# Optimization experiments

Hardware: AMD Instinct MI355X
Metric: run time of the kernel (lower is better)

Reference implementation:

```python
import jax, jax.numpy as jnp
import numpy as np

N, E, F, H = 50000, 500000, 128, 128   # nodes, edges, in-features, hidden
L, R, B = 3, 8, 30                     # layers, relations, bases
G, C = 16, 8                           # graphs in batch, classes
EPS = 1e-5


def setup_inputs() -> dict:
    key = jax.random.key(0)
    ks = jax.random.split(key, 16)
    x = jax.random.normal(ks[0], (N, F), jnp.float32)
    edge_index = jax.random.randint(ks[1], (2, E), 0, N)
    edge_attr = jax.random.randint(ks[2], (E,), 0, R)
    batch = jnp.sort(jax.random.randint(ks[3], (N,), 0, G))
    # RGCN params (all layers share shapes since F == H)
    basis = jax.random.normal(ks[4], (L, B, H, H), jnp.float32) * 0.05
    comp = jax.random.normal(ks[5], (L, R, B), jnp.float32) * 0.2
    root = jax.random.normal(ks[6], (L, H, H), jnp.float32) * 0.05
    bias = jnp.zeros((L, H), jnp.float32)
    # BatchNorm (eval mode: running stats)
    bn1_gamma = jnp.ones((F,), jnp.float32)
    bn1_beta = jnp.zeros((F,), jnp.float32)
    bn1_mean = jax.random.normal(ks[7], (F,), jnp.float32) * 0.1
    bn1_var = jax.random.uniform(ks[8], (F,), jnp.float32, 0.5, 1.5)
    bn2_gamma = jnp.ones((H,), jnp.float32)
    bn2_beta = jnp.zeros((H,), jnp.float32)
    bn2_mean = jax.random.normal(ks[9], (H,), jnp.float32) * 0.1
    bn2_var = jax.random.uniform(ks[10], (H,), jnp.float32, 0.5, 1.5)
    fc1_w = jax.random.normal(ks[11], (H, H), jnp.float32) * 0.05
    fc1_b = jnp.zeros((H,), jnp.float32)
    fc2_w = jax.random.normal(ks[12], (H, C), jnp.float32) * 0.05
    fc2_b = jnp.zeros((C,), jnp.float32)
    return dict(x=x, edge_index=edge_index, edge_attr=edge_attr, batch=batch,
                bn1_gamma=bn1_gamma, bn1_beta=bn1_beta, bn1_mean=bn1_mean, bn1_var=bn1_var,
                basis=basis, comp=comp, root=root, bias=bias,
                bn2_gamma=bn2_gamma, bn2_beta=bn2_beta, bn2_mean=bn2_mean, bn2_var=bn2_var,
                fc1_w=fc1_w, fc1_b=fc1_b, fc2_w=fc2_w, fc2_b=fc2_b)


def _bn(x, gamma, beta, mean, var):
    return (x - mean) * jax.lax.rsqrt(var + EPS) * gamma + beta


def _rgcn_layer(x, basis_l, comp_l, root_l, bias_l, src, dst, edge_attr):
    # root transform + bias
    out = x @ root_l + bias_l
    # relation-wise basis-decomposed message passing, mean-aggregated per relation
    for r in range(R):
        W_r = jnp.einsum('b,bio->io', comp_l[r], basis_l)  # [H, H]
        xw = x @ W_r                                       # [N, H]
        mask = (edge_attr == r).astype(x.dtype)            # [E]
        msg = xw[src] * mask[:, None]                      # gather + mask
        agg = jax.ops.segment_sum(msg, dst, num_segments=N)
        deg = jax.ops.segment_sum(mask, dst, num_segments=N)
        out = out + agg / jnp.maximum(deg, 1.0)[:, None]
    return out


def reference(x, edge_index, edge_attr, batch,
              bn1_gamma, bn1_beta, bn1_mean, bn1_var,
              basis, comp, root, bias,
              bn2_gamma, bn2_beta, bn2_mean, bn2_var,
              fc1_w, fc1_b, fc2_w, fc2_b):
    src, dst = edge_index[0], edge_index[1]
    h = _bn(x, bn1_gamma, bn1_beta, bn1_mean, bn1_var)
    for l in range(L):
        h = jax.nn.relu(_rgcn_layer(h, basis[l], comp[l], root[l], bias[l], src, dst, edge_attr))
        # dropout is identity in eval mode
    # global mean pool per graph
    sums = jax.ops.segment_sum(h, batch, num_segments=G)            # [G, H]
    counts = jax.ops.segment_sum(jnp.ones((N,), h.dtype), batch, num_segments=G)
    g = sums / jnp.maximum(counts, 1.0)[:, None]
    g = _bn(g, bn2_gamma, bn2_beta, bn2_mean, bn2_var)
    # temporal_type == 'mean'
    v = jax.nn.relu(g.mean(axis=0))                                 # [H]
    v = jax.nn.relu(v @ fc1_w + fc1_b)
    logits = v @ fc2_w + fc2_b                                      # [C]
    return jax.nn.log_softmax(logits, axis=-1)
```

## Files before the change

### kernel.cpp

```cpp
#include <hip/hip_runtime.h>
#include <hip/hip_bf16.h>

#define NN 50000
#define NE 500000
#define HID 128
#define LAYERS 3
#define RELS 8
#define BASES 30
#define GRAPHS 16
#define CLASSES 8
#define EPSV 1e-5f
#define NOUT (HID * (RELS + 1))
#define SCAN_CHUNK 1024
#define SCAN_NBLK ((NN + SCAN_CHUNK - 1) / SCAN_CHUNK)
#define PCHUNK 128
#define NSTRIPE ((NN + 127) / 128)
#define NSG ((NSTRIPE + 7) / 8)

typedef __attribute__((ext_vector_type(8))) short short8;
typedef __attribute__((ext_vector_type(4))) float f32x4;
typedef __attribute__((ext_vector_type(2))) float f32x2;

__device__ __forceinline__ float bf2f(unsigned short u) {
    union { unsigned int i; float f; } x; x.i = ((unsigned int)u) << 16; return x.f;
}
__device__ __forceinline__ unsigned short f2bf(float f) {
    __hip_bfloat16 b = __float2bfloat16(f);
    return *(unsigned short*)&b;
}
template <bool HI>
__device__ __forceinline__ f32x2 fp8x2_2f(int u) {
    return __builtin_amdgcn_cvt_pk_f32_fp8(u, HI);
}
__device__ __forceinline__ int permf(int f) {
    return (f & 64) | ((f & 15) << 2) | ((f >> 4) & 3);
}
__device__ __forceinline__ int ipermf(int q) {
    return (q & 64) | ((q & 3) << 4) | ((q >> 2) & 15);
}

__global__ __launch_bounds__(256) void build_wcat(const float* __restrict__ basis,
                                                  const float* __restrict__ comp,
                                                  const float* __restrict__ root,
                                                  unsigned short* __restrict__ wT) {
    int bid = blockIdx.x;
    int l = bid >> 6;
    int k0 = (bid & 63) << 1;
    __shared__ float cl[RELS * BASES];
    int tid = threadIdx.x;
    if (tid < RELS * BASES) cl[tid] = comp[l * RELS * BASES + tid];
    __syncthreads();
    int j = tid & 127;
    int k = k0 + (tid >> 7);
    int pk = permf(k);
    const float* bp = basis + ((size_t)l * BASES * HID + k) * HID + j;
    float acc[RELS];
#pragma unroll
    for (int r = 0; r < RELS; ++r) acc[r] = 0.f;
    for (int b = 0; b < BASES; ++b) {
        float v = bp[(size_t)b * HID * HID];
#pragma unroll
        for (int r = 0; r < RELS; ++r) acc[r] += cl[r * BASES + b] * v;
    }
    unsigned short* wl = wT + (size_t)l * NOUT * HID;
#pragma unroll
    for (int r = 0; r < RELS; ++r)
        wl[(size_t)((1 + r) * HID + j) * HID + pk] = f2bf(acc[r]);
    wl[(size_t)j * HID + pk] = f2bf(root[((size_t)l * HID + k) * HID + j]);
}

__global__ void bn1_kernel(const float* __restrict__ x, const float* __restrict__ gamma,
                           const float* __restrict__ beta, const float* __restrict__ mean,
                           const float* __restrict__ var, unsigned short* __restrict__ habf) {
    int idx = blockIdx.x * blockDim.x + threadIdx.x;
    if (idx >= NN * HID) return;
    int q = idx & (HID - 1);
    int n = idx >> 7;
    int f = ipermf(q);
    habf[idx] = f2bf((x[(n << 7) + f] - mean[f]) * rsqrtf(var[f] + EPSV) * gamma[f] + beta[f]);
}

__global__ void deg_kernel(const int* __restrict__ ei, const int* __restrict__ ea,
                           float* __restrict__ deg) {
    int e = blockIdx.x * blockDim.x + threadIdx.x;
    if (e >= NE) return;
    int dst = ei[NE + e];
    atomicAdd(&deg[(size_t)dst * RELS + ea[e]], 1.0f);
}

__global__ void invdeg_kernel(float* __restrict__ deg, int* __restrict__ degi) {
    int n = blockIdx.x * blockDim.x + threadIdx.x;
    if (n >= NN) return;
    float s = 0.f;
#pragma unroll
    for (int r = 0; r < RELS; ++r) {
        float d = deg[(size_t)n * RELS + r];
        s += d;
        deg[(size_t)n * RELS + r] = 1.0f / fmaxf(d, 1.0f);
    }
    degi[n] = (int)(s + 0.5f);
}

__global__ __launch_bounds__(256) void scan_partial(const int* __restrict__ degi,
                                                    int* __restrict__ rowptr,
                                                    int* __restrict__ bsum) {
    __shared__ int ssc[256];
    int t = threadIdx.x;
    int base = blockIdx.x * SCAN_CHUNK + t * 4;
    int v[4];
#pragma unroll
    for (int j = 0; j < 4; ++j) v[j] = (base + j < NN) ? degi[base + j] : 0;
    int tsum = v[0] + v[1] + v[2] + v[3];
    ssc[t] = tsum;
    __syncthreads();
    for (int ofs = 1; ofs < 256; ofs <<= 1) {
        int add = (t >= ofs) ? ssc[t - ofs] : 0;
        __syncthreads();
        ssc[t] += add;
        __syncthreads();
    }
    int excl = ssc[t] - tsum;
    int e = 0;
#pragma unroll
    for (int j = 0; j < 4; ++j) {
        if (base + j < NN) rowptr[base + j] = excl + e;
        e += v[j];
    }
    if (t == 255) bsum[blockIdx.x] = ssc[255];
}

__global__ void scan_bsum(int* __restrict__ bsum) {
    if (threadIdx.x == 0) {
        int acc = 0;
        for (int b = 0; b < SCAN_NBLK; ++b) { int v = bsum[b]; bsum[b] = acc; acc += v; }
    }
}

__global__ __launch_bounds__(256) void scan_add(int* __restrict__ rowptr,
                                                const int* __restrict__ bsum) {
    int i = blockIdx.x * blockDim.x + threadIdx.x;
    if (i < NN) rowptr[i] += bsum[i >> 10];
    if (i == 0) rowptr[NN] = NE;
}

__global__ void fill_kernel(const int* __restrict__ ei, const int* __restrict__ ea,
                            const int* __restrict__ rowptr, const float* __restrict__ invdeg,
                            int* __restrict__ fillcnt, int* __restrict__ epk,
                            float* __restrict__ escale) {
    int e = blockIdx.x * blockDim.x + threadIdx.x;
    if (e >= NE) return;
    int src = ei[e];
    int dst = ei[NE + e];
    int r = ea[e];
    int pos = atomicAdd(&fillcnt[dst], 1);
    int slot = rowptr[dst] + pos;
    epk[slot] = src | (r << 20);
    escale[slot] = invdeg[(size_t)dst * RELS + r];
}

__global__ __launch_bounds__(256) void gemm_mfma(const unsigned short* __restrict__ habf,
                                                 const unsigned short* __restrict__ wT,
                                                 const float* __restrict__ bias,
                                                 unsigned short* __restrict__ hnb,
                                                 unsigned char* __restrict__ xwb) {
    __shared__ __align__(16) unsigned short As[128][72];
    __shared__ __align__(16) unsigned short Bs[128][72];
    int bid = blockIdx.x;
    int sm8 = bid & 7;
    int rest = bid >> 3;
    int n0 = rest % (RELS + 1);
    int g = rest / (RELS + 1);
    int stripe = g * 8 + sm8;
    if (stripe >= NSTRIPE) return;
    int row0 = stripe * 128;

    int tid = threadIdx.x;
    int wave = tid >> 6, lane = tid & 63;
    int wm = (wave & 1) * 64, wn = (wave >> 1) * 64;
    int quad = lane >> 4, l16 = lane & 15;

    f32x4 acc[4][4];
#pragma unroll
    for (int i = 0; i < 4; ++i)
#pragma unroll
        for (int j = 0; j < 4; ++j) acc[i][j] = (f32x4){0.f, 0.f, 0.f, 0.f};

    int srow = tid >> 1;
    int shalf = (tid & 1) * 32;
    for (int k0 = 0; k0 < HID; k0 += 64) {
        int grow = row0 + srow;
        const uint4* ga = (const uint4*)(habf + (size_t)grow * HID + k0 + shalf);
        const uint4* gb = (const uint4*)(wT + (size_t)(n0 * 128 + srow) * HID + k0 + shalf);
        uint4 z = {0u, 0u, 0u, 0u};
#pragma unroll
        for (int c = 0; c < 4; ++c) {
            *(uint4*)&As[srow][shalf + c * 8] = (grow < NN) ? ga[c] : z;
            *(uint4*)&Bs[srow][shalf + c * 8] = gb[c];
        }
        __syncthreads();
#pragma unroll
        for (int kc = 0; kc < 2; ++kc) {
            int ko = kc * 32 + quad * 8;
            short8 a[4], b[4];
#pragma unroll
            for (int i = 0; i < 4; ++i) {
                a[i] = *(const short8*)&As[wm + i * 16 + l16][ko];
                b[i] = *(const short8*)&Bs[wn + i * 16 + l16][ko];
            }
#pragma unroll
            for (int i = 0; i < 4; ++i)
#pragma unroll
                for (int j = 0; j < 4; ++j)
                    acc[i][j] = __builtin_amdgcn_mfma_f32_16x16x32_bf16(a[i], b[j], acc[i][j], 0, 0, 0);
        }
        __syncthreads();
    }

    int pbase = wn + l16 * 4;
    if (n0 == 0) {
#pragma unroll
        for (int i = 0; i < 4; ++i)
#pragma unroll
            for (int reg = 0; reg < 4; ++reg) {
                int grow = row0 + wm + i * 16 + quad * 4 + reg;
                if (grow >= NN) continue;
                unsigned lo = (unsigned)f2bf(acc[i][0][reg] + bias[wn + l16]) |
                              ((unsigned)f2bf(acc[i][1][reg] + bias[wn + 16 + l16]) << 16);
                unsigned hi = (unsigned)f2bf(acc[i][2][reg] + bias[wn + 32 + l16]) |
                              ((unsigned)f2bf(acc[i][3][reg] + bias[wn + 48 + l16]) << 16);
                uint2 pk = {lo, hi};
                *(uint2*)(hnb + (size_t)grow * HID + pbase) = pk;
            }
    } else {
        int cbase = (n0 - 1) * 128;
#pragma unroll
        for (int i = 0; i < 4; ++i)
#pragma unroll
            for (int reg = 0; reg < 4; ++reg) {
                int grow = row0 + wm + i * 16 + quad * 4 + reg;
                if (grow >= NN) continue;
                unsigned w = (unsigned)__builtin_amdgcn_cvt_pk_fp8_f32(acc[i][0][reg], acc[i][1][reg], 0, false);
                w = (unsigned)__builtin_amdgcn_cvt_pk_fp8_f32(acc[i][2][reg], acc[i][3][reg], (int)w, true);
                *(unsigned*)(xwb + (size_t)grow * (RELS * HID) + cbase + pbase) = w;
            }
    }
}

__global__ __launch_bounds__(256) void aggregate_kernel(const int* __restrict__ rowptr,
                                                        const int* __restrict__ epk,
                                                        const float* __restrict__ escale,
                                                        const unsigned char* __restrict__ xwb,
                                                        const unsigned short* __restrict__ hnb,
                                                        unsigned short* __restrict__ habf) {
    int lane = threadIdx.x & 63;
    int half = lane >> 5;
    int hl = lane & 31;
    int node = (blockIdx.x << 3) + ((threadIdx.x >> 6) << 1) + half;
    if (node >= NN) return;
    int beg = rowptr[node], end = rowptr[node + 1];
    float a0 = 0.f, a1 = 0.f, a2 = 0.f, a3 = 0.f;
    for (int b0 = beg; b0 < end; b0 += 32) {
        int cnt = min(32, end - b0);
        int myp = 0; float mys = 0.f;
        if (hl < cnt) { myp = epk[b0 + hl]; mys = escale[b0 + hl]; }
        int sbase = half << 5;
        int j = 0;
        for (; j + 2 <= cnt; j += 2) {
            int p0 = __shfl(myp, sbase + j);
            int p1 = __shfl(myp, sbase + j + 1);
            float s0 = __shfl(mys, sbase + j);
            float s1 = __shfl(mys, sbase + j + 1);
            unsigned u0 = *(const unsigned*)(xwb + (size_t)(p0 & 0xFFFFF) * (RELS * HID) + (p0 >> 20) * HID + hl * 4);
            unsigned u1 = *(const unsigned*)(xwb + (size_t)(p1 & 0xFFFFF) * (RELS * HID) + (p1 >> 20) * HID + hl * 4);
            f32x2 l0 = fp8x2_2f<false>((int)u0), h0 = fp8x2_2f<true>((int)u0);
            f32x2 l1 = fp8x2_2f<false>((int)u1), h1 = fp8x2_2f<true>((int)u1);
            a0 += l0.x * s0 + l1.x * s1;
            a1 += l0.y * s0 + l1.y * s1;
            a2 += h0.x * s0 + h1.x * s1;
            a3 += h0.y * s0 + h1.y * s1;
        }
        for (; j < cnt; ++j) {
            int p = __shfl(myp, sbase + j);
            float s = __shfl(mys, sbase + j);
            unsigned u = *(const unsigned*)(xwb + (size_t)(p & 0xFFFFF) * (RELS * HID) + (p >> 20) * HID + hl * 4);
            f32x2 lo = fp8x2_2f<false>((int)u), hi = fp8x2_2f<true>((int)u);
            a0 += lo.x * s; a1 += lo.y * s; a2 += hi.x * s; a3 += hi.y * s;
        }
    }
    const ushort2* hp = (const ushort2*)(hnb + (size_t)node * HID + hl * 4);
    ushort2 c0 = hp[0], c1 = hp[1];
    ushort2 o0, o1;
    o0.x = f2bf(fmaxf(bf2f(c0.x) + a0, 0.f));
    o0.y = f2bf(fmaxf(bf2f(c0.y) + a1, 0.f));
    o1.x = f2bf(fmaxf(bf2f(c1.x) + a2, 0.f));
    o1.y = f2bf(fmaxf(bf2f(c1.y) + a3, 0.f));
    ushort2* op = (ushort2*)(habf + (size_t)node * HID + hl * 4);
    op[0] = o0;
    op[1] = o1;
}

__global__ __launch_bounds__(256) void pool_kernel(const unsigned short* __restrict__ habf,
                                                   const int* __restrict__ batch,
                                                   float* __restrict__ psum,
                                                   float* __restrict__ pcnt) {
    int tid = threadIdx.x;
    int f = tid & 127;
    int sub = tid >> 7;
    int base = blockIdx.x * PCHUNK;
    float acc = 0.f, cnt = 0.f;
    int gcur = -1;
    for (int it = 0; it < PCHUNK / 2; ++it) {
        int node = base + it * 2 + sub;
        if (node >= NN) break;
        int g = batch[node];
        if (g != gcur) {
            if (gcur >= 0) {
                atomicAdd(&psum[gcur * HID + f], acc);
                if (f == 0) atomicAdd(&pcnt[gcur], cnt);
            }
            gcur = g; acc = 0.f; cnt = 0.f;
        }
        acc += bf2f(habf[(size_t)node * HID + f]);
        cnt += 1.f;
    }
    if (gcur >= 0) {
        atomicAdd(&psum[gcur * HID + f], acc);
        if (f == 0) atomicAdd(&pcnt[gcur], cnt);
    }
}

__global__ void head_kernel(const float* __restrict__ psum, const float* __restrict__ pcnt,
                            const float* __restrict__ g2, const float* __restrict__ b2,
                            const float* __restrict__ m2, const float* __restrict__ v2,
                            const float* __restrict__ fc1w, const float* __restrict__ fc1b,
                            const float* __restrict__ fc2w, const float* __restrict__ fc2b,
                            float* __restrict__ out) {
    __shared__ float v[HID];
    __shared__ float u[HID];
    __shared__ float lg[CLASSES];
    int j = threadIdx.x;
    int pj = permf(j);
    float acc = 0.f;
    for (int g = 0; g < GRAPHS; ++g) {
        float val = psum[g * HID + pj] / fmaxf(pcnt[g], 1.0f);
        val = (val - m2[j]) * rsqrtf(v2[j] + EPSV) * g2[j] + b2[j];
        acc += val;
    }
    v[j] = fmaxf(acc / (float)GRAPHS, 0.f);
    __syncthreads();
    float s = fc1b[j];
    for (int k = 0; k < HID; ++k) s += v[k] * fc1w[k * HID + j];
    u[j] = fmaxf(s, 0.f);
    __syncthreads();
    if (j < CLASSES) {
        float t = fc2b[j];
        for (int k = 0; k < HID; ++k) t += u[k] * fc2w[k * CLASSES + j];
        lg[j] = t;
    }
    __syncthreads();
    if (j < CLASSES) {
        float mx = lg[0];
        for (int c = 1; c < CLASSES; ++c) mx = fmaxf(mx, lg[c]);
        float se = 0.f;
        for (int c = 0; c < CLASSES; ++c) se += expf(lg[c] - mx);
        out[j] = lg[j] - mx - logf(se);
    }
}

extern "C" void kernel_launch(void* const* d_in, const int* in_sizes, int n_in,
                              void* d_out, int out_size, void* d_ws, size_t ws_size,
                              hipStream_t stream) {
    const float* x     = (const float*)d_in[0];
    const int*   ei    = (const int*)d_in[1];
    const int*   ea    = (const int*)d_in[2];
    const int*   batch = (const int*)d_in[3];
    const float* bn1g  = (const float*)d_in[4];
    const float* bn1b  = (const float*)d_in[5];
    const float* bn1m  = (const float*)d_in[6];
    const float* bn1v  = (const float*)d_in[7];
    const float* basis = (const float*)d_in[8];
    const float* comp  = (const float*)d_in[9];
    const float* root  = (const float*)d_in[10];
    const float* bias  = (const float*)d_in[11];
    const float* bn2g  = (const float*)d_in[12];
    const float* bn2b  = (const float*)d_in[13];
    const float* bn2m  = (const float*)d_in[14];
    const float* bn2v  = (const float*)d_in[15];
    const float* fc1w  = (const float*)d_in[16];
    const float* fc1b  = (const float*)d_in[17];
    const float* fc2w  = (const float*)d_in[18];
    const float* fc2b  = (const float*)d_in[19];

    float* ws = (float*)d_ws;
    size_t off = 0;
    unsigned short* wT = (unsigned short*)(ws + off); off += (size_t)LAYERS * NOUT * HID / 2;
    unsigned short* hnb  = (unsigned short*)(ws + off); off += (size_t)NN * HID / 2;
    unsigned short* habf = (unsigned short*)(ws + off); off += (size_t)NN * HID / 2;
    float* deg    = ws + off; off += (size_t)NN * RELS;
    float* psum   = ws + off; off += (size_t)GRAPHS * HID + GRAPHS;
    float* pcnt   = psum + GRAPHS * HID;
    float* escale = ws + off; off += (size_t)NE;
    int* degi     = (int*)(ws + off); off += (size_t)NN;
    int* rowptr   = (int*)(ws + off); off += (size_t)NN + 1;
    int* fillcnt  = (int*)(ws + off); off += (size_t)NN;
    int* bsum     = (int*)(ws + off); off += (size_t)SCAN_NBLK;
    int* epk      = (int*)(ws + off); off += (size_t)NE;
    off = (off + 3) & ~(size_t)3;
    unsigned char* xwb = (unsigned char*)(ws + off);
    off += (size_t)NN * RELS * HID / 4;
    if (ws_size < off * sizeof(float)) return;

    hipMemsetAsync(psum, 0, (GRAPHS * HID + GRAPHS) * sizeof(float), stream);
    hipMemsetAsync(deg, 0, (size_t)NN * RELS * sizeof(float), stream);
    hipMemsetAsync(fillcnt, 0, (size_t)NN * sizeof(int), stream);

    build_wcat<<<LAYERS * 64, 256, 0, stream>>>(basis, comp, root, wT);
    bn1_kernel<<<(NN * HID + 255) / 256, 256, 0, stream>>>(x, bn1g, bn1b, bn1m, bn1v, habf);

    deg_kernel<<<(NE + 255) / 256, 256, 0, stream>>>(ei, ea, deg);
    invdeg_kernel<<<(NN + 255) / 256, 256, 0, stream>>>(deg, degi);
    scan_partial<<<SCAN_NBLK, 256, 0, stream>>>(degi, rowptr, bsum);
    scan_bsum<<<1, 64, 0, stream>>>(bsum);
    scan_add<<<(NN + 255) / 256, 256, 0, stream>>>(rowptr, bsum);
    fill_kernel<<<(NE + 255) / 256, 256, 0, stream>>>(ei, ea, rowptr, deg, fillcnt, epk, escale);

    int gblocks = NSG * (RELS + 1) * 8;
    for (int l = 0; l < LAYERS; ++l) {
        gemm_mfma<<<gblocks, 256, 0, stream>>>(habf, wT + (size_t)l * NOUT * HID,
                                               bias + (size_t)l * HID, hnb, xwb);
        aggregate_kernel<<<(NN + 7) / 8, 256, 0, stream>>>(rowptr, epk, escale, xwb, hnb, habf);
    }

    pool_kernel<<<(NN + PCHUNK - 1) / PCHUNK, 256, 0, stream>>>(habf, batch, psum, pcnt);
    head_kernel<<<1, 128, 0, stream>>>(psum, pcnt, bn2g, bn2b, bn2m, bn2v,
                                       fc1w, fc1b, fc2w, fc2b, (float*)d_out);
}
```

Measured before the change: 433.0 us.

## Use direct global-to-LDS loads in GEMM and fetch inverse degree per relation via shuffles

The GEMM now loads the full 128x128 A and B tiles into LDS in one pass using global_load_lds with an XOR swizzle, replacing the two-step register-staged K loop and halving the barriers. The per-edge escale array is removed: each aggregation lane loads the node's per-relation inverse degree once and edges read it with a shuffle indexed by relation. The edge loop is unrolled by 4 to keep more gathers in flight. LDS use per GEMM block grows to 64 KB, which may lower occupancy, and the extra shuffles add instruction cost.

```diff
diff --git a/kernel.cpp b/kernel.cpp
--- a/kernel.cpp
+++ b/kernel.cpp
@@ -38,6 +38,11 @@
 __device__ __forceinline__ int ipermf(int q) {
     return (q & 64) | ((q & 3) << 4) | ((q >> 2) & 15);
 }
+__device__ __forceinline__ void gload16(const void* g, void* l) {
+    __builtin_amdgcn_global_load_lds(
+        (const __attribute__((address_space(1))) unsigned int*)g,
+        (__attribute__((address_space(3))) unsigned int*)l, 16, 0, 0);
+}
 
 __global__ __launch_bounds__(256) void build_wcat(const float* __restrict__ basis,
                                                   const float* __restrict__ comp,
@@ -144,18 +149,15 @@
 }
 
 __global__ void fill_kernel(const int* __restrict__ ei, const int* __restrict__ ea,
-                            const int* __restrict__ rowptr, const float* __restrict__ invdeg,
-                            int* __restrict__ fillcnt, int* __restrict__ epk,
-                            float* __restrict__ escale) {
+                            const int* __restrict__ rowptr,
+                            int* __restrict__ fillcnt, int* __restrict__ epk) {
     int e = blockIdx.x * blockDim.x + threadIdx.x;
     if (e >= NE) return;
     int src = ei[e];
     int dst = ei[NE + e];
     int r = ea[e];
     int pos = atomicAdd(&fillcnt[dst], 1);
-    int slot = rowptr[dst] + pos;
-    epk[slot] = src | (r << 20);
-    escale[slot] = invdeg[(size_t)dst * RELS + r];
+    epk[rowptr[dst] + pos] = src | (r << 20);
 }
 
 __global__ __launch_bounds__(256) void gemm_mfma(const unsigned short* __restrict__ habf,
@@ -163,8 +165,8 @@
                                                  const float* __restrict__ bias,
                                                  unsigned short* __restrict__ hnb,
                                                  unsigned char* __restrict__ xwb) {
-    __shared__ __align__(16) unsigned short As[128][72];
-    __shared__ __align__(16) unsigned short Bs[128][72];
+    __shared__ __align__(16) unsigned short As[128 * HID];
+    __shared__ __align__(16) unsigned short Bs[128 * HID];
     int bid = blockIdx.x;
     int sm8 = bid & 7;
     int rest = bid >> 3;
@@ -179,41 +181,41 @@
     int wm = (wave & 1) * 64, wn = (wave >> 1) * 64;
     int quad = lane >> 4, l16 = lane & 15;
 
+    int sr = lane >> 4;
+    int sp = lane & 15;
+#pragma unroll
+    for (int q = 0; q < 8; ++q) {
+        int rb = wave * 32 + q * 4;
+        int r = rb + sr;
+        int sc = (sp ^ (r & 7)) << 3;
+        int ga = row0 + r; if (ga > NN - 1) ga = NN - 1;
+        gload16(habf + (size_t)ga * HID + sc, &As[rb * HID]);
+        gload16(wT + (size_t)(n0 * 128 + r) * HID + sc, &Bs[rb * HID]);
+    }
+
     f32x4 acc[4][4];
 #pragma unroll
     for (int i = 0; i < 4; ++i)
 #pragma unroll
         for (int j = 0; j < 4; ++j) acc[i][j] = (f32x4){0.f, 0.f, 0.f, 0.f};
 
-    int srow = tid >> 1;
-    int shalf = (tid & 1) * 32;
-    for (int k0 = 0; k0 < HID; k0 += 64) {
-        int grow = row0 + srow;
-        const uint4* ga = (const uint4*)(habf + (size_t)grow * HID + k0 + shalf);
-        const uint4* gb = (const uint4*)(wT + (size_t)(n0 * 128 + srow) * HID + k0 + shalf);
-        uint4 z = {0u, 0u, 0u, 0u};
-#pragma unroll
-        for (int c = 0; c < 4; ++c) {
-            *(uint4*)&As[srow][shalf + c * 8] = (grow < NN) ? ga[c] : z;
-            *(uint4*)&Bs[srow][shalf + c * 8] = gb[c];
+    __syncthreads();
+
+    int sx = l16 & 7;
+#pragma unroll
+    for (int kc = 0; kc < 4; ++kc) {
+        int ca = ((kc * 4 + quad) ^ sx) << 3;
+        short8 a[4], b[4];
+#pragma unroll
+        for (int i = 0; i < 4; ++i) {
+            a[i] = *(const short8*)&As[(wm + i * 16 + l16) * HID + ca];
+            b[i] = *(const short8*)&Bs[(wn + i * 16 + l16) * HID + ca];
         }
-        __syncthreads();
-#pragma unroll
-        for (int kc = 0; kc < 2; ++kc) {
-            int ko = kc * 32 + quad * 8;
-            short8 a[4], b[4];
-#pragma unroll
-            for (int i = 0; i < 4; ++i) {
-                a[i] = *(const short8*)&As[wm + i * 16 + l16][ko];
-                b[i] = *(const short8*)&Bs[wn + i * 16 + l16][ko];
-            }
-#pragma unroll
-            for (int i = 0; i < 4; ++i)
-#pragma unroll
-                for (int j = 0; j < 4; ++j)
-                    acc[i][j] = __builtin_amdgcn_mfma_f32_16x16x32_bf16(a[i], b[j], acc[i][j], 0, 0, 0);
-        }
-        __syncthreads();
+#pragma unroll
+        for (int i = 0; i < 4; ++i)
+#pragma unroll
+            for (int j = 0; j < 4; ++j)
+                acc[i][j] = __builtin_amdgcn_mfma_f32_16x16x32_bf16(a[i], b[j], acc[i][j], 0, 0, 0);
     }
 
     int pbase = wn + l16 * 4;
@@ -248,7 +250,7 @@
 
 __global__ __launch_bounds__(256) void aggregate_kernel(const int* __restrict__ rowptr,
                                                         const int* __restrict__ epk,
-                                                        const float* __restrict__ escale,
+                                                        const float* __restrict__ invdeg,
                                                         const unsigned char* __restrict__ xwb,
                                                         const unsigned short* __restrict__ hnb,
                                                         unsigned short* __restrict__ habf) {
@@ -258,30 +260,39 @@
     int node = (blockIdx.x << 3) + ((threadIdx.x >> 6) << 1) + half;
     if (node >= NN) return;
     int beg = rowptr[node], end = rowptr[node + 1];
+    float dv = invdeg[(size_t)node * RELS + (hl & 7)];
     float a0 = 0.f, a1 = 0.f, a2 = 0.f, a3 = 0.f;
     for (int b0 = beg; b0 < end; b0 += 32) {
         int cnt = min(32, end - b0);
-        int myp = 0; float mys = 0.f;
-        if (hl < cnt) { myp = epk[b0 + hl]; mys = escale[b0 + hl]; }
+        int myp = 0;
+        if (hl < cnt) myp = epk[b0 + hl];
         int sbase = half << 5;
         int j = 0;
-        for (; j + 2 <= cnt; j += 2) {
+        for (; j + 4 <= cnt; j += 4) {
             int p0 = __shfl(myp, sbase + j);
             int p1 = __shfl(myp, sbase + j + 1);
-            float s0 = __shfl(mys, sbase + j);
-            float s1 = __shfl(mys, sbase + j + 1);
+            int p2 = __shfl(myp, sbase + j + 2);
+            int p3 = __shfl(myp, sbase + j + 3);
+            float s0 = __shfl(dv, sbase + (p0 >> 20));
+            float s1 = __shfl(dv, sbase + (p1 >> 20));
+            float s2 = __shfl(dv, sbase + (p2 >> 20));
+            float s3 = __shfl(dv, sbase + (p3 >> 20));
             unsigned u0 = *(const unsigned*)(xwb + (size_t)(p0 & 0xFFFFF) * (RELS * HID) + (p0 >> 20) * HID + hl * 4);
             unsigned u1 = *(const unsigned*)(xwb + (size_t)(p1 & 0xFFFFF) * (RELS * HID) + (p1 >> 20) * HID + hl * 4);
+            unsigned u2 = *(const unsigned*)(xwb + (size_t)(p2 & 0xFFFFF) * (RELS * HID) + (p2 >> 20) * HID + hl * 4);
+            unsigned u3 = *(const unsigned*)(xwb + (size_t)(p3 & 0xFFFFF) * (RELS * HID) + (p3 >> 20) * HID + hl * 4);
             f32x2 l0 = fp8x2_2f<false>((int)u0), h0 = fp8x2_2f<true>((int)u0);
             f32x2 l1 = fp8x2_2f<false>((int)u1), h1 = fp8x2_2f<true>((int)u1);
-            a0 += l0.x * s0 + l1.x * s1;
-            a1 += l0.y * s0 + l1.y * s1;
-            a2 += h0.x * s0 + h1.x * s1;
-            a3 += h0.y * s0 + h1.y * s1;
+            f32x2 l2 = fp8x2_2f<false>((int)u2), h2 = fp8x2_2f<true>((int)u2);
+            f32x2 l3 = fp8x2_2f<false>((int)u3), h3 = fp8x2_2f<true>((int)u3);
+            a0 += l0.x * s0 + l1.x * s1 + l2.x * s2 + l3.x * s3;
+            a1 += l0.y * s0 + l1.y * s1 + l2.y * s2 + l3.y * s3;
+            a2 += h0.x * s0 + h1.x * s1 + h2.x * s2 + h3.x * s3;
+            a3 += h0.y * s0 + h1.y * s1 + h2.y * s2 + h3.y * s3;
         }
         for (; j < cnt; ++j) {
             int p = __shfl(myp, sbase + j);
-            float s = __shfl(mys, sbase + j);
+            float s = __shfl(dv, sbase + (p >> 20));
             unsigned u = *(const unsigned*)(xwb + (size_t)(p & 0xFFFFF) * (RELS * HID) + (p >> 20) * HID + hl * 4);
             f32x2 lo = fp8x2_2f<false>((int)u), hi = fp8x2_2f<true>((int)u);
             a0 += lo.x * s; a1 += lo.y * s; a2 += hi.x * s; a3 += hi.y * s;
@@ -399,7 +410,6 @@
     float* deg    = ws + off; off += (size_t)NN * RELS;
     float* psum   = ws + off; off += (size_t)GRAPHS * HID + GRAPHS;
     float* pcnt   = psum + GRAPHS * HID;
-    float* escale = ws + off; off += (size_t)NE;
     int* degi     = (int*)(ws + off); off += (size_t)NN;
     int* rowptr   = (int*)(ws + off); off += (size_t)NN + 1;
     int* fillcnt  = (int*)(ws + off); off += (size_t)NN;
@@ -422,13 +432,13 @@
     scan_partial<<<SCAN_NBLK, 256, 0, stream>>>(degi, rowptr, bsum);
     scan_bsum<<<1, 64, 0, stream>>>(bsum);
     scan_add<<<(NN + 255) / 256, 256, 0, stream>>>(rowptr, bsum);
-    fill_kernel<<<(NE + 255) / 256, 256, 0, stream>>>(ei, ea, rowptr, deg, fillcnt, epk, escale);
+    fill_kernel<<<(NE + 255) / 256, 256, 0, stream>>>(ei, ea, rowptr, fillcnt, epk);
 
     int gblocks = NSG * (RELS + 1) * 8;
     for (int l = 0; l < LAYERS; ++l) {
         gemm_mfma<<<gblocks, 256, 0, stream>>>(habf, wT + (size_t)l * NOUT * HID,
                                                bias + (size_t)l * HID, hnb, xwb);
-        aggregate_kernel<<<(NN + 7) / 8, 256, 0, stream>>>(rowptr, epk, escale, xwb, hnb, habf);
+        aggregate_kernel<<<(NN + 7) / 8, 256, 0, stream>>>(rowptr, epk, deg, xwb, hnb, habf);
     }
 
     pool_kernel<<<(NN + PCHUNK - 1) / PCHUNK, 256, 0, stream>>>(habf, batch, psum, pcnt);
```

After: 406.9 us. 1.06x faster.
